# Kernel optimization log

Measured on AMD Instinct MI355X. Metric: run time of the kernel, lower is better.

The kernel has to match this reference:

```python
import jax, jax.numpy as jnp
import numpy as np

B, H, W, C, NBHD, T, OUT_DIM = 4, 96, 96, 256, 48, 3025, 512
N = H * W
INNER = 4
DS_RATE = 0.25


def _layer_norm(x, w, b, eps=1e-5):
    mu = jnp.mean(x, axis=-1, keepdims=True)
    var = jnp.mean((x - mu) ** 2, axis=-1, keepdims=True)
    return (x - mu) * jax.lax.rsqrt(var + eps) * w + b


def setup_inputs() -> dict:
    key = jax.random.key(0)
    ks = jax.random.split(key, 8)
    # regular grid positions: pos % 4 == 0 (both dims) on exactly 24*24=576 tokens
    yy, xx = jnp.meshgrid(jnp.arange(H), jnp.arange(W), indexing='ij')
    pos = jnp.stack([yy, xx], axis=-1).reshape(1, N, 2).astype(jnp.float32)
    pos = jnp.broadcast_to(pos, (B, N, 2))
    feat = jax.random.normal(ks[0], (B, N, C), dtype=jnp.float32)
    member_idx = jax.random.randint(ks[1], (B, N, NBHD), 0, N)
    cluster_mask = (jax.random.uniform(ks[2], (B, N, NBHD)) > 0.1).astype(jnp.float32)
    learned_prob = jax.random.uniform(ks[3], (B, N, 1), dtype=jnp.float32)
    pe_idx = jax.random.randint(ks[4], (B, N, NBHD), 0, T)
    pre_table = jax.random.normal(ks[5], (T, 5), dtype=jnp.float32)
    # weight_net: Linear(5,4) + LayerNorm(4) + GELU
    w1 = jax.random.normal(ks[6], (5, INNER), dtype=jnp.float32) * 0.3
    b1 = jnp.zeros((INNER,), jnp.float32)
    ln1_w = jnp.ones((INNER,), jnp.float32)
    ln1_b = jnp.zeros((INNER,), jnp.float32)
    # norm over inner_ch*dim, then Linear(inner_ch*dim -> out_dim)
    norm_w = jnp.ones((INNER * C,), jnp.float32)
    norm_b = jnp.zeros((INNER * C,), jnp.float32)
    lin_w = jax.random.normal(ks[7], (INNER * C, OUT_DIM), dtype=jnp.float32) * 0.02
    lin_b = jnp.zeros((OUT_DIM,), jnp.float32)
    return {
        'pos': pos, 'feat': feat, 'member_idx': member_idx,
        'cluster_mask': cluster_mask, 'learned_prob': learned_prob,
        'pe_idx': pe_idx, 'pre_table': pre_table,
        'w1': w1, 'b1': b1, 'ln1_w': ln1_w, 'ln1_b': ln1_b,
        'norm_w': norm_w, 'norm_b': norm_b, 'lin_w': lin_w, 'lin_b': lin_b,
        'stride': 2, 'reserve_num': 576,
    }


def reference(pos, feat, member_idx, cluster_mask, learned_prob, pe_idx,
              pre_table, w1, b1, ln1_w, ln1_b, norm_w, norm_b, lin_w, lin_b,
              stride, reserve_num):
    b, n, c = feat.shape
    nbhd = member_idx.shape[-1]
    keep_num = int(n * DS_RATE)
    sample_num = keep_num - reserve_num

    pos_long = pos.astype(jnp.int32)
    lp_det = jax.lax.stop_gradient(learned_prob[..., 0])  # b x n (detached in torch)
    reserve_mask = jnp.all(pos_long % (stride * 2) == 0, axis=-1).astype(jnp.float32)
    final_prob = lp_det + reserve_mask * (-100.0)

    # topk sampled tokens (reserved tokens pushed to -100 so never sampled)
    sample_idx = jax.lax.top_k(final_prob, sample_num)[1]  # b x sample_num
    # reserved token indices in ascending index order (torch nonzero order)
    reserve_idx = jnp.argsort(-reserve_mask, axis=1, stable=True)[:, :reserve_num]
    idx = jnp.concatenate([sample_idx, reserve_idx], axis=1)  # b x keep_num

    pos_down = jnp.take_along_axis(pos, idx[:, :, None], axis=1)  # b x keep x 2

    member_d = jnp.take_along_axis(member_idx, idx[:, :, None], axis=1)   # b x keep x nbhd
    pe_d = jnp.take_along_axis(pe_idx, idx[:, :, None], axis=1)
    cmask_d = jnp.take_along_axis(cluster_mask, idx[:, :, None], axis=1)

    flat_mi = member_d.reshape(b, keep_num * nbhd)
    # gather learned prob of each neighbor (NOT detached: grads flow)
    lp_nb = jnp.take_along_axis(learned_prob, flat_mi[:, :, None], axis=1)
    lp_nb = lp_nb.reshape(b, keep_num, nbhd, 1)

    # weight_net over pre-computed position table -> T x inner_ch
    wt = jax.nn.gelu(_layer_norm(pre_table @ w1 + b1, ln1_w, ln1_b))
    weights = wt[pe_d]  # b x keep x nbhd x inner_ch
    weights = weights * (lp_nb * cmask_d[..., None])

    # gather neighbor features and do position-weighted aggregation
    feat_g = jnp.take_along_axis(feat, flat_mi[:, :, None], axis=1)
    feat_g = feat_g.reshape(b, keep_num, nbhd, c)
    feat_down = jnp.einsum('bnkm,bnkc->bnmc', weights, feat_g)
    feat_down = feat_down.reshape(b, keep_num, INNER * c)

    feat_down = _layer_norm(feat_down, norm_w, norm_b)
    feat_down = feat_down @ lin_w + lin_b
    return pos_down, feat_down
```

## Files before the change

### kernel.cpp

```cpp
#include <hip/hip_runtime.h>
#include <hip/hip_bf16.h>
#include <stdint.h>

#define BB 4
#define NN 9216
#define CC 256
#define NBHD 48
#define T_TAB 3025
#define OUT_DIM 512
#define KEEP 2304
#define RESERVE 576
#define SAMPLE 1728
#define W_IMG 96
#define CAND_CAP 6144

typedef __attribute__((ext_vector_type(4))) float f32x4;
typedef __attribute__((ext_vector_type(8))) short s16x8;

__device__ inline unsigned short f2bf_bits(float x) {
    __hip_bfloat16 h = __float2bfloat16(x);
    return __builtin_bit_cast(unsigned short, h);
}

__device__ inline unsigned int fkey(float v) {
    unsigned int u = __builtin_bit_cast(unsigned int, v);
    return (u & 0x80000000u) ? ~u : (u | 0x80000000u);
}
__device__ inline float final_prob_val(const float* lpb, int i) {
    int y = i / W_IMG, x = i % W_IMG;
    bool res = ((y & 3) == 0) && ((x & 3) == 0);
    return lpb[i] + (res ? -100.0f : 0.0f);
}

__global__ __launch_bounds__(256) void prep_kernel(
        const float* __restrict__ W, __hip_bfloat16* __restrict__ Wt,
        const float* __restrict__ pre_table,
        const float* __restrict__ w1, const float* __restrict__ b1,
        const float* __restrict__ ln1w, const float* __restrict__ ln1b,
        float* __restrict__ wt) {
    if (blockIdx.x < 512) {
        __shared__ float s[32][33];
        int bx = blockIdx.x & 15;
        int by = blockIdx.x >> 4;
        int tx = threadIdx.x & 31, ty = threadIdx.x >> 5;
#pragma unroll
        for (int r = 0; r < 4; r++)
            s[ty * 4 + r][tx] = W[(size_t)(by * 32 + ty * 4 + r) * 512 + bx * 32 + tx];
        __syncthreads();
#pragma unroll
        for (int r = 0; r < 4; r++)
            Wt[(size_t)(bx * 32 + ty * 4 + r) * 1024 + by * 32 + tx] =
                __float2bfloat16(s[tx][ty * 4 + r]);
        return;
    }
    int t = (blockIdx.x - 512) * 256 + threadIdx.x;
    if (t >= T_TAB) return;
    float p[5];
#pragma unroll
    for (int j = 0; j < 5; j++) p[j] = pre_table[t * 5 + j];
    float h[4];
#pragma unroll
    for (int m = 0; m < 4; m++) {
        float a = b1[m];
#pragma unroll
        for (int j = 0; j < 5; j++) a += p[j] * w1[j * 4 + m];
        h[m] = a;
    }
    float mu = 0.25f * (h[0] + h[1] + h[2] + h[3]);
    float var = 0.f;
#pragma unroll
    for (int m = 0; m < 4; m++) { float d = h[m] - mu; var += d * d; }
    var *= 0.25f;
    float rs = rsqrtf(var + 1e-5f);
#pragma unroll
    for (int m = 0; m < 4; m++) {
        float x = (h[m] - mu) * rs * ln1w[m] + ln1b[m];
        float u = 0.7978845608028654f * (x + 0.044715f * x * x * x);
        wt[t * 4 + m] = 0.5f * x * (1.0f + tanhf(u));
    }
}

__global__ void hist_kernel(const float* __restrict__ lp,
                            int* __restrict__ hist) {
    int g = blockIdx.x * 256 + threadIdx.x;
    if (g >= BB * NN) return;
    int b = g / NN, i = g % NN;
    float v = final_prob_val(lp + b * NN, i);
    unsigned int bin = fkey(v) >> 16;
    atomicAdd(&hist[b * 65536 + bin], 1);
}

__global__ __launch_bounds__(256) void thresh_kernel(const int* __restrict__ hist,
                                                     int* __restrict__ thr) {
    int b = blockIdx.x, t = threadIdx.x;
    __shared__ int s_scan[256];
    __shared__ int s_rc, s_ex;
    const int* h = hist + b * 65536;
    int lo = 65536 - (t + 1) * 256;
    const int4* h4 = (const int4*)(h + lo);
    int sum = 0;
#pragma unroll 8
    for (int k = 0; k < 64; k++) {
        int4 v = h4[k];
        sum += v.x + v.y + v.z + v.w;
    }
    int own = sum;
    s_scan[t] = sum;
    __syncthreads();
    for (int off = 1; off < 256; off <<= 1) {
        int add = (t >= off) ? s_scan[t - off] : 0;
        __syncthreads();
        s_scan[t] += add;
        __syncthreads();
    }
    int incl = s_scan[t], ex = incl - own;
    if (ex < SAMPLE && incl >= SAMPLE) { s_rc = t; s_ex = ex; }
    __syncthreads();
    int rc = s_rc, ex0 = s_ex;
    int bin = 65536 - rc * 256 - 1 - t;
    int own2 = h[bin];
    s_scan[t] = own2;
    __syncthreads();
    for (int off = 1; off < 256; off <<= 1) {
        int add = (t >= off) ? s_scan[t - off] : 0;
        __syncthreads();
        s_scan[t] += add;
        __syncthreads();
    }
    int incl2 = ex0 + s_scan[t], ex2 = incl2 - own2;
    if (ex2 < SAMPLE && incl2 >= SAMPLE) thr[b] = bin;
}

__global__ __launch_bounds__(256) void collect_kernel(
        const float* __restrict__ lp,
        const int* __restrict__ thr,
        int* __restrict__ cnt,
        unsigned long long* __restrict__ candk,
        int* __restrict__ idx,
        float* __restrict__ pos_down) {
    __shared__ int s_wcnt[4];
    __shared__ int s_base;
    int g = blockIdx.x * 256 + threadIdx.x;
    int b = g / NN, i = g % NN;
    int lane = threadIdx.x & 63, wave = threadIdx.x >> 6;
    int y = i / W_IMG, x = i % W_IMG;
    bool res = ((y & 3) == 0) && ((x & 3) == 0);
    float v = lp[g];
    bool pred = false;
    if (res) {
        int slot = SAMPLE + (y >> 2) * (W_IMG / 4) + (x >> 2);
        idx[b * KEEP + slot] = i;
        pos_down[(b * KEEP + slot) * 2 + 0] = (float)y;
        pos_down[(b * KEEP + slot) * 2 + 1] = (float)x;
    } else {
        pred = ((int)(fkey(v) >> 16) >= thr[b]);
    }
    unsigned long long m = __ballot(pred);
    int wcount = __popcll(m);
    int lpos = __popcll(m & ((1ull << lane) - 1ull));
    if (lane == 0) s_wcnt[wave] = wcount;
    __syncthreads();
    if (threadIdx.x == 0) {
        int tot = s_wcnt[0] + s_wcnt[1] + s_wcnt[2] + s_wcnt[3];
        s_base = atomicAdd(&cnt[b], tot);
    }
    __syncthreads();
    if (pred) {
        int off = s_base + lpos;
        for (int w = 0; w < wave; w++) off += s_wcnt[w];
        if (off < CAND_CAP)
            candk[b * CAND_CAP + off] =
                ((unsigned long long)fkey(v) << 32) | (unsigned int)(NN - 1 - i);
    }
}

#define RCHUNK 2048
__global__ __launch_bounds__(256) void rank_cand_kernel(
        const int* __restrict__ cnt,
        const unsigned long long* __restrict__ candk,
        int* __restrict__ idx,
        float* __restrict__ pos_down) {
    __shared__ unsigned long long sk[RCHUNK];
    int b = blockIdx.y;
    int C = cnt[b]; if (C > CAND_CAP) C = CAND_CAP;
    if ((int)(blockIdx.x * 256) >= C) return;
    int i = blockIdx.x * 256 + threadIdx.x;
    bool valid = (i < C);
    unsigned long long ki = valid ? candk[b * CAND_CAP + i] : 0ull;
    int rank = 0;
    for (int base = 0; base < C; base += RCHUNK) {
        int len = min(RCHUNK, C - base);
        for (int j = threadIdx.x; j < len; j += 256)
            sk[j] = candk[b * CAND_CAP + base + j];
        __syncthreads();
        if (valid) {
            int j = 0;
            for (; j + 16 <= len; j += 16) {
#pragma unroll
                for (int u = 0; u < 16; u++)
                    rank += (int)(sk[j + u] > ki);
            }
            for (; j < len; j++) rank += (int)(sk[j] > ki);
        }
        __syncthreads();
    }
    if (valid && rank < SAMPLE) {
        int ii = NN - 1 - (int)(ki & 0xffffffffULL);
        idx[b * KEEP + rank] = ii;
        pos_down[(b * KEEP + rank) * 2 + 0] = (float)(ii / W_IMG);
        pos_down[(b * KEEP + rank) * 2 + 1] = (float)(ii % W_IMG);
    }
}

__global__ void feat2bf_kernel(const float* __restrict__ f,
                               unsigned short* __restrict__ o) {
    int g = blockIdx.x * 256 + threadIdx.x;
    float4 v = ((const float4*)f)[g];
    ushort4 u;
    u.x = f2bf_bits(v.x); u.y = f2bf_bits(v.y);
    u.z = f2bf_bits(v.z); u.w = f2bf_bits(v.w);
    ((ushort4*)o)[g] = u;
}

__device__ inline float ldf(const float* p) { return *p; }
__device__ inline float ldf(const __hip_bfloat16* p) { return __bfloat162float(*p); }

template <typename FT>
__global__ __launch_bounds__(256) void agg_kernel(
        const FT* __restrict__ feat,
        const int* __restrict__ member_idx,
        const float* __restrict__ cmask,
        const float* __restrict__ lp,
        const int* __restrict__ pe_idx,
        const float* __restrict__ wt,
        const int* __restrict__ idx,
        const float* __restrict__ norm_w,
        const float* __restrict__ norm_b,
        __hip_bfloat16* __restrict__ xnorm) {
    int t = blockIdx.x, b = blockIdx.y, tid = threadIdx.x;
    __shared__ int s_mem[NBHD];
    __shared__ float s_w[NBHD * 4];
    __shared__ float s_red[8];
    int i = idx[b * KEEP + t];
    if (tid < NBHD) {
        size_t base = ((size_t)b * NN + i) * NBHD + tid;
        int mi = member_idx[base];
        int pe = pe_idx[base];
        float fsc = lp[b * NN + mi] * cmask[base];
        s_mem[tid] = mi;
        s_w[tid * 4 + 0] = wt[pe * 4 + 0] * fsc;
        s_w[tid * 4 + 1] = wt[pe * 4 + 1] * fsc;
        s_w[tid * 4 + 2] = wt[pe * 4 + 2] * fsc;
        s_w[tid * 4 + 3] = wt[pe * 4 + 3] * fsc;
    }
    __syncthreads();
    float a0 = 0.f, a1 = 0.f, a2 = 0.f, a3 = 0.f;
    const FT* fb = feat + (size_t)b * NN * CC + tid;
#pragma unroll 4
    for (int k = 0; k < NBHD; k++) {
        float fv = ldf(fb + (size_t)s_mem[k] * CC);
        a0 += s_w[k * 4 + 0] * fv;
        a1 += s_w[k * 4 + 1] * fv;
        a2 += s_w[k * 4 + 2] * fv;
        a3 += s_w[k * 4 + 3] * fv;
    }
    float s1 = a0 + a1 + a2 + a3;
    float s2 = a0 * a0 + a1 * a1 + a2 * a2 + a3 * a3;
    for (int off = 32; off > 0; off >>= 1) {
        s1 += __shfl_down(s1, off);
        s2 += __shfl_down(s2, off);
    }
    int wid = tid >> 6;
    if ((tid & 63) == 0) { s_red[wid] = s1; s_red[4 + wid] = s2; }
    __syncthreads();
    float S1 = s_red[0] + s_red[1] + s_red[2] + s_red[3];
    float S2 = s_red[4] + s_red[5] + s_red[6] + s_red[7];
    float mu = S1 * (1.0f / 1024.0f);
    float var = S2 * (1.0f / 1024.0f) - mu * mu;
    float rs = rsqrtf(var + 1e-5f);
    __hip_bfloat16* xo = xnorm + ((size_t)(b * KEEP + t)) * 1024;
#pragma unroll
    for (int m = 0; m < 4; m++) {
        float am = (m == 0) ? a0 : (m == 1) ? a1 : (m == 2) ? a2 : a3;
        int c = m * 256 + tid;
        xo[c] = __float2bfloat16((am - mu) * rs * norm_w[c] + norm_b[c]);
    }
}

__device__ inline void async16(const void* g, void* l) {
    __builtin_amdgcn_global_load_lds(
        (const __attribute__((address_space(1))) void*)g,
        (__attribute__((address_space(3))) void*)l, 16, 0, 0);
}
__device__ inline void mfma16x16x32(f32x4& d, const s16x8& a, const s16x8& b) {
    asm("v_mfma_f32_16x16x32_bf16 %0, %1, %2, %0" : "+v"(d) : "v"(a), "v"(b));
}

__global__ __launch_bounds__(256) void mfma_gemm(
        const __hip_bfloat16* __restrict__ A,
        const __hip_bfloat16* __restrict__ Bt,
        const float* __restrict__ bias,
        float* __restrict__ Cout) {
    __shared__ __hip_bfloat16 sA[128 * 32];
    __shared__ __hip_bfloat16 sB[128 * 32];
    int tid = threadIdx.x;
    int wave = tid >> 6, lane = tid & 63;
    int wm = wave >> 1, wn = wave & 1;
    int row0 = blockIdx.y * 128, col0 = blockIdx.x * 128;

    int lrow = lane >> 2;
    int lcol = (lane & 3) * 8;
    const __hip_bfloat16* gA = A + (size_t)(row0 + wave * 32 + lrow) * 1024 + lcol;
    const __hip_bfloat16* gB = Bt + (size_t)(col0 + wave * 32 + lrow) * 1024 + lcol;
    __hip_bfloat16* lA0 = sA + (wave * 32) * 32;
    __hip_bfloat16* lA1 = sA + (wave * 32 + 16) * 32;
    __hip_bfloat16* lB0 = sB + (wave * 32) * 32;
    __hip_bfloat16* lB1 = sB + (wave * 32 + 16) * 32;

    f32x4 acc[4][4] = {};
    int fr = lane & 15;
    int fq = lane >> 4;

    for (int kk = 0; kk < 1024; kk += 32) {
        async16(gA + kk, lA0);
        async16(gA + kk + 16 * 1024, lA1);
        async16(gB + kk, lB0);
        async16(gB + kk + 16 * 1024, lB1);
        __syncthreads();
        s16x8 af[4], bf[4];
#pragma unroll
        for (int i = 0; i < 4; i++)
            af[i] = *(const s16x8*)(sA + (wm * 64 + i * 16 + fr) * 32 + fq * 8);
#pragma unroll
        for (int j = 0; j < 4; j++)
            bf[j] = *(const s16x8*)(sB + (wn * 64 + j * 16 + fr) * 32 + fq * 8);
#pragma unroll
        for (int i = 0; i < 4; i++)
#pragma unroll
            for (int j = 0; j < 4; j++)
                mfma16x16x32(acc[i][j], af[i], bf[j]);
        __syncthreads();
    }
    asm volatile("s_nop 7\ns_nop 7" ::);
    float bv[4];
#pragma unroll
    for (int j = 0; j < 4; j++) bv[j] = bias[col0 + wn * 64 + j * 16 + fr];
#pragma unroll
    for (int i = 0; i < 4; i++) {
        int row = row0 + wm * 64 + i * 16 + fq * 4;
#pragma unroll
        for (int j = 0; j < 4; j++) {
            int col = col0 + wn * 64 + j * 16 + fr;
            float* cp = Cout + (size_t)row * 512 + col;
#pragma unroll
            for (int r = 0; r < 4; r++)
                cp[(size_t)r * 512] = acc[i][j][r] + bv[j];
        }
    }
}

extern "C" void kernel_launch(void* const* d_in, const int* in_sizes, int n_in,
                              void* d_out, int out_size, void* d_ws, size_t ws_size,
                              hipStream_t stream) {
    const float* pos       = (const float*)d_in[0];
    const float* feat      = (const float*)d_in[1];
    const int*   member_idx= (const int*)d_in[2];
    const float* cmask     = (const float*)d_in[3];
    const float* lp        = (const float*)d_in[4];
    const int*   pe_idx    = (const int*)d_in[5];
    const float* pre_table = (const float*)d_in[6];
    const float* w1        = (const float*)d_in[7];
    const float* b1        = (const float*)d_in[8];
    const float* ln1w      = (const float*)d_in[9];
    const float* ln1b      = (const float*)d_in[10];
    const float* norm_w    = (const float*)d_in[11];
    const float* norm_b    = (const float*)d_in[12];
    const float* lin_w     = (const float*)d_in[13];
    const float* lin_b     = (const float*)d_in[14];

    float* out = (float*)d_out;
    float* pos_down = out;
    float* feat_out = out + (size_t)BB * KEEP * 2;

    char* ws = (char*)d_ws;
    float*              wt     = (float*)(ws + 0);
    int*                hist   = (int*)  (ws + 48640);
    int*                ccnt   = (int*)  (ws + 1097216);
    int*                thr    = (int*)  (ws + 1097472);
    unsigned long long* candk  = (unsigned long long*)(ws + 1097728);
    int*                idx    = (int*)  (ws + 1294336);
    __hip_bfloat16*     wtb    = (__hip_bfloat16*)(ws + 1331200);
    __hip_bfloat16*     xnormb = (__hip_bfloat16*)(ws + 2379776);
    __hip_bfloat16*     featb  = (__hip_bfloat16*)(ws + 21254144);
    const size_t NEED_BF16FEAT = 21254144 + 18874368;
    bool use_bf16_feat = (ws_size >= NEED_BF16FEAT);

    prep_kernel<<<dim3(512 + (T_TAB + 255) / 256), 256, 0, stream>>>(
        lin_w, wtb, pre_table, w1, b1, ln1w, ln1b, wt);
    hipMemsetAsync(hist, 0, 1048576 + 256, stream);
    hist_kernel<<<dim3((BB * NN) / 256), 256, 0, stream>>>(lp, hist);
    thresh_kernel<<<dim3(BB), 256, 0, stream>>>(hist, thr);
    collect_kernel<<<dim3((BB * NN) / 256), 256, 0, stream>>>(lp, thr, ccnt, candk, idx, pos_down);
    rank_cand_kernel<<<dim3(CAND_CAP / 256, BB), 256, 0, stream>>>(ccnt, candk, idx, pos_down);
    if (use_bf16_feat) {
        feat2bf_kernel<<<dim3((BB * NN * CC / 4) / 256), 256, 0, stream>>>(feat, (unsigned short*)featb);
        agg_kernel<__hip_bfloat16><<<dim3(KEEP, BB), 256, 0, stream>>>(
            featb, member_idx, cmask, lp, pe_idx, wt, idx, norm_w, norm_b, xnormb);
    } else {
        agg_kernel<float><<<dim3(KEEP, BB), 256, 0, stream>>>(
            feat, member_idx, cmask, lp, pe_idx, wt, idx, norm_w, norm_b, xnormb);
    }
    mfma_gemm<<<dim3(OUT_DIM / 128, (BB * KEEP) / 128), 256, 0, stream>>>(xnormb, wtb, lin_b, feat_out);
}
```

Before: 240.1 us.

## Fuse prep/hist/bf16 kernels and split neighbor loop across waves in agg

Merges the weight table prep, histogram and feature-to-bf16 conversion into one launch, which removes two kernel launches. The histogram now runs before thresh with the conversion overlapped. The aggregation kernel is restructured so that each wave handles 12 of the 48 neighbors. Each lane loads 4 contiguous bf16 channels with one 8-byte load, and the partial sums are reduced through shared memory. The block index is remapped to interleave batches. The fallback path used when the workspace is too small for bf16 features is dropped, which assumes that space is always available.

After: 227.9 us. 1.05x faster.

```diff
diff --git a/kernel.cpp b/kernel.cpp
--- a/kernel.cpp
+++ b/kernel.cpp
@@ -37,7 +37,9 @@
         const float* __restrict__ pre_table,
         const float* __restrict__ w1, const float* __restrict__ b1,
         const float* __restrict__ ln1w, const float* __restrict__ ln1b,
-        float* __restrict__ wt) {
+        float* __restrict__ wt,
+        const float* __restrict__ lp, int* __restrict__ hist,
+        const float* __restrict__ feat, unsigned short* __restrict__ featb) {
     if (blockIdx.x < 512) {
         __shared__ float s[32][33];
         int bx = blockIdx.x & 15;
@@ -53,41 +55,50 @@
                 __float2bfloat16(s[tx][ty * 4 + r]);
         return;
     }
-    int t = (blockIdx.x - 512) * 256 + threadIdx.x;
-    if (t >= T_TAB) return;
-    float p[5];
-#pragma unroll
-    for (int j = 0; j < 5; j++) p[j] = pre_table[t * 5 + j];
-    float h[4];
-#pragma unroll
-    for (int m = 0; m < 4; m++) {
-        float a = b1[m];
-#pragma unroll
-        for (int j = 0; j < 5; j++) a += p[j] * w1[j * 4 + m];
-        h[m] = a;
-    }
-    float mu = 0.25f * (h[0] + h[1] + h[2] + h[3]);
-    float var = 0.f;
-#pragma unroll
-    for (int m = 0; m < 4; m++) { float d = h[m] - mu; var += d * d; }
-    var *= 0.25f;
-    float rs = rsqrtf(var + 1e-5f);
-#pragma unroll
-    for (int m = 0; m < 4; m++) {
-        float x = (h[m] - mu) * rs * ln1w[m] + ln1b[m];
-        float u = 0.7978845608028654f * (x + 0.044715f * x * x * x);
-        wt[t * 4 + m] = 0.5f * x * (1.0f + tanhf(u));
-    }
-}
-
-__global__ void hist_kernel(const float* __restrict__ lp,
-                            int* __restrict__ hist) {
-    int g = blockIdx.x * 256 + threadIdx.x;
-    if (g >= BB * NN) return;
-    int b = g / NN, i = g % NN;
-    float v = final_prob_val(lp + b * NN, i);
-    unsigned int bin = fkey(v) >> 16;
-    atomicAdd(&hist[b * 65536 + bin], 1);
+    if (blockIdx.x < 524) {
+        int t = (blockIdx.x - 512) * 256 + threadIdx.x;
+        if (t >= T_TAB) return;
+        float p[5];
+#pragma unroll
+        for (int j = 0; j < 5; j++) p[j] = pre_table[t * 5 + j];
+        float h[4];
+#pragma unroll
+        for (int m = 0; m < 4; m++) {
+            float a = b1[m];
+#pragma unroll
+            for (int j = 0; j < 5; j++) a += p[j] * w1[j * 4 + m];
+            h[m] = a;
+        }
+        float mu = 0.25f * (h[0] + h[1] + h[2] + h[3]);
+        float var = 0.f;
+#pragma unroll
+        for (int m = 0; m < 4; m++) { float d = h[m] - mu; var += d * d; }
+        var *= 0.25f;
+        float rs = rsqrtf(var + 1e-5f);
+#pragma unroll
+        for (int m = 0; m < 4; m++) {
+            float x = (h[m] - mu) * rs * ln1w[m] + ln1b[m];
+            float u = 0.7978845608028654f * (x + 0.044715f * x * x * x);
+            wt[t * 4 + m] = 0.5f * x * (1.0f + tanhf(u));
+        }
+        return;
+    }
+    if (blockIdx.x < 668) {
+        int g = (blockIdx.x - 524) * 256 + threadIdx.x;
+        int b = g / NN, i = g % NN;
+        float v = final_prob_val(lp + b * NN, i);
+        unsigned int bin = fkey(v) >> 16;
+        atomicAdd(&hist[b * 65536 + bin], 1);
+        return;
+    }
+    {
+        int g = (blockIdx.x - 668) * 256 + threadIdx.x;
+        float4 v = ((const float4*)feat)[g];
+        ushort4 u;
+        u.x = f2bf_bits(v.x); u.y = f2bf_bits(v.y);
+        u.z = f2bf_bits(v.z); u.w = f2bf_bits(v.w);
+        ((ushort4*)featb)[g] = u;
+    }
 }
 
 __global__ __launch_bounds__(256) void thresh_kernel(const int* __restrict__ hist,
@@ -212,22 +223,9 @@
     }
 }
 
-__global__ void feat2bf_kernel(const float* __restrict__ f,
-                               unsigned short* __restrict__ o) {
-    int g = blockIdx.x * 256 + threadIdx.x;
-    float4 v = ((const float4*)f)[g];
-    ushort4 u;
-    u.x = f2bf_bits(v.x); u.y = f2bf_bits(v.y);
-    u.z = f2bf_bits(v.z); u.w = f2bf_bits(v.w);
-    ((ushort4*)o)[g] = u;
-}
-
-__device__ inline float ldf(const float* p) { return *p; }
-__device__ inline float ldf(const __hip_bfloat16* p) { return __bfloat162float(*p); }
-
-template <typename FT>
+#define ASTRIDE 20
 __global__ __launch_bounds__(256) void agg_kernel(
-        const FT* __restrict__ feat,
+        const __hip_bfloat16* __restrict__ feat,
         const int* __restrict__ member_idx,
         const float* __restrict__ cmask,
         const float* __restrict__ lp,
@@ -237,9 +235,13 @@
         const float* __restrict__ norm_w,
         const float* __restrict__ norm_b,
         __hip_bfloat16* __restrict__ xnorm) {
-    int t = blockIdx.x, b = blockIdx.y, tid = threadIdx.x;
+    int L = blockIdx.x;
+    int b = (L >> 1) & 3;
+    int t = (L >> 3) * 2 + (L & 1);
+    int tid = threadIdx.x;
     __shared__ int s_mem[NBHD];
     __shared__ float s_w[NBHD * 4];
+    __shared__ float s_part[4 * 64 * ASTRIDE];
     __shared__ float s_red[8];
     int i = idx[b * KEEP + t];
     if (tid < NBHD) {
@@ -254,15 +256,35 @@
         s_w[tid * 4 + 3] = wt[pe * 4 + 3] * fsc;
     }
     __syncthreads();
+    int wave = tid >> 6, lane = tid & 63;
+    const __hip_bfloat16* fbase = feat + (size_t)b * NN * CC;
+    float acc[4][4] = {};
+#pragma unroll
+    for (int j = 0; j < 12; j++) {
+        int k = wave * 12 + j;
+        int mi = s_mem[k];
+        float4 w4 = *(const float4*)&s_w[k * 4];
+        uint2 v = *((const uint2*)(fbase + (size_t)mi * CC) + lane);
+        float f0 = __builtin_bit_cast(float, v.x << 16);
+        float f1 = __builtin_bit_cast(float, v.x & 0xffff0000u);
+        float f2 = __builtin_bit_cast(float, v.y << 16);
+        float f3 = __builtin_bit_cast(float, v.y & 0xffff0000u);
+        acc[0][0] += w4.x * f0; acc[0][1] += w4.x * f1; acc[0][2] += w4.x * f2; acc[0][3] += w4.x * f3;
+        acc[1][0] += w4.y * f0; acc[1][1] += w4.y * f1; acc[1][2] += w4.y * f2; acc[1][3] += w4.y * f3;
+        acc[2][0] += w4.z * f0; acc[2][1] += w4.z * f1; acc[2][2] += w4.z * f2; acc[2][3] += w4.z * f3;
+        acc[3][0] += w4.w * f0; acc[3][1] += w4.w * f1; acc[3][2] += w4.w * f2; acc[3][3] += w4.w * f3;
+    }
+    float* pp = &s_part[(wave * 64 + lane) * ASTRIDE];
+#pragma unroll
+    for (int m = 0; m < 4; m++)
+        *(float4*)(pp + m * 4) = make_float4(acc[m][0], acc[m][1], acc[m][2], acc[m][3]);
+    __syncthreads();
+    int cl = tid >> 2, cc = tid & 3;
     float a0 = 0.f, a1 = 0.f, a2 = 0.f, a3 = 0.f;
-    const FT* fb = feat + (size_t)b * NN * CC + tid;
-#pragma unroll 4
-    for (int k = 0; k < NBHD; k++) {
-        float fv = ldf(fb + (size_t)s_mem[k] * CC);
-        a0 += s_w[k * 4 + 0] * fv;
-        a1 += s_w[k * 4 + 1] * fv;
-        a2 += s_w[k * 4 + 2] * fv;
-        a3 += s_w[k * 4 + 3] * fv;
+#pragma unroll
+    for (int w = 0; w < 4; w++) {
+        const float* q = &s_part[(w * 64 + cl) * ASTRIDE + cc];
+        a0 += q[0]; a1 += q[4]; a2 += q[8]; a3 += q[12];
     }
     float s1 = a0 + a1 + a2 + a3;
     float s2 = a0 * a0 + a1 * a1 + a2 * a2 + a3 * a3;
@@ -279,12 +301,10 @@
     float var = S2 * (1.0f / 1024.0f) - mu * mu;
     float rs = rsqrtf(var + 1e-5f);
     __hip_bfloat16* xo = xnorm + ((size_t)(b * KEEP + t)) * 1024;
-#pragma unroll
-    for (int m = 0; m < 4; m++) {
-        float am = (m == 0) ? a0 : (m == 1) ? a1 : (m == 2) ? a2 : a3;
-        int c = m * 256 + tid;
-        xo[c] = __float2bfloat16((am - mu) * rs * norm_w[c] + norm_b[c]);
-    }
+    xo[0 * 256 + tid] = __float2bfloat16((a0 - mu) * rs * norm_w[0 * 256 + tid] + norm_b[0 * 256 + tid]);
+    xo[1 * 256 + tid] = __float2bfloat16((a1 - mu) * rs * norm_w[1 * 256 + tid] + norm_b[1 * 256 + tid]);
+    xo[2 * 256 + tid] = __float2bfloat16((a2 - mu) * rs * norm_w[2 * 256 + tid] + norm_b[2 * 256 + tid]);
+    xo[3 * 256 + tid] = __float2bfloat16((a3 - mu) * rs * norm_w[3 * 256 + tid] + norm_b[3 * 256 + tid]);
 }
 
 __device__ inline void async16(const void* g, void* l) {
@@ -392,23 +412,15 @@
     __hip_bfloat16*     wtb    = (__hip_bfloat16*)(ws + 1331200);
     __hip_bfloat16*     xnormb = (__hip_bfloat16*)(ws + 2379776);
     __hip_bfloat16*     featb  = (__hip_bfloat16*)(ws + 21254144);
-    const size_t NEED_BF16FEAT = 21254144 + 18874368;
-    bool use_bf16_feat = (ws_size >= NEED_BF16FEAT);
-
-    prep_kernel<<<dim3(512 + (T_TAB + 255) / 256), 256, 0, stream>>>(
-        lin_w, wtb, pre_table, w1, b1, ln1w, ln1b, wt);
+
     hipMemsetAsync(hist, 0, 1048576 + 256, stream);
-    hist_kernel<<<dim3((BB * NN) / 256), 256, 0, stream>>>(lp, hist);
+    prep_kernel<<<dim3(512 + 12 + 144 + (BB * NN * CC / 4) / 256), 256, 0, stream>>>(
+        lin_w, wtb, pre_table, w1, b1, ln1w, ln1b, wt, lp, hist,
+        feat, (unsigned short*)featb);
     thresh_kernel<<<dim3(BB), 256, 0, stream>>>(hist, thr);
     collect_kernel<<<dim3((BB * NN) / 256), 256, 0, stream>>>(lp, thr, ccnt, candk, idx, pos_down);
     rank_cand_kernel<<<dim3(CAND_CAP / 256, BB), 256, 0, stream>>>(ccnt, candk, idx, pos_down);
-    if (use_bf16_feat) {
-        feat2bf_kernel<<<dim3((BB * NN * CC / 4) / 256), 256, 0, stream>>>(feat, (unsigned short*)featb);
-        agg_kernel<__hip_bfloat16><<<dim3(KEEP, BB), 256, 0, stream>>>(
-            featb, member_idx, cmask, lp, pe_idx, wt, idx, norm_w, norm_b, xnormb);
-    } else {
-        agg_kernel<float><<<dim3(KEEP, BB), 256, 0, stream>>>(
-            feat, member_idx, cmask, lp, pe_idx, wt, idx, norm_w, norm_b, xnormb);
-    }
+    agg_kernel<<<dim3(BB * KEEP), 256, 0, stream>>>(
+        featb, member_idx, cmask, lp, pe_idx, wt, idx, norm_w, norm_b, xnormb);
     mfma_gemm<<<dim3(OUT_DIM / 128, (BB * KEEP) / 128), 256, 0, stream>>>(xnormb, wtb, lin_b, feat_out);
 }
```
